# Optimization experiments

Hardware: AMD Instinct MI355X
Metric: run time of the kernel (lower is better)

## Reference

```python
import jax, jax.numpy as jnp
import numpy as np

N = 50000      # nodes
E = 800000     # edges
D = 128        # in_channels
H = 128        # hidden_channels
G = 64         # graphs in batch
OUT = 10       # out_channels
L = 6          # gcn layers (hardcoded in module)
EPS = 1e-5     # batchnorm eps


def setup_inputs() -> dict:
    key = jax.random.key(0)
    ks = jax.random.split(key, 8)
    s = 1.0 / np.sqrt(H)
    return {
        "x": jax.random.normal(ks[0], (N, D), jnp.float32),
        "edge_index": jax.random.randint(ks[1], (2, E), 0, N),
        "batch": jnp.sort(jax.random.randint(ks[2], (N,), 0, G)),
        "conv_W": jax.random.normal(ks[3], (L, D, H), jnp.float32) * s,
        "conv_b": jnp.zeros((L, H), jnp.float32),
        "bn_gamma": jnp.ones((L - 1, H), jnp.float32),
        "bn_beta": jnp.zeros((L - 1, H), jnp.float32),
        "head_W1": jax.random.normal(ks[4], (H, H), jnp.float32) * s,
        "head_b1": jnp.zeros((H,), jnp.float32),
        "head_bn_gamma": jnp.ones((H,), jnp.float32),
        "head_bn_beta": jnp.zeros((H,), jnp.float32),
        "head_W2": jax.random.normal(ks[5], (H, H), jnp.float32) * s,
        "head_b2": jnp.zeros((H,), jnp.float32),
        "head_W3": jax.random.normal(ks[6], (H, OUT), jnp.float32) * s,
        "head_b3": jnp.zeros((OUT,), jnp.float32),
    }


def _batchnorm(h, gamma, beta):
    # track_running_stats=False -> always batch statistics, biased variance
    mu = h.mean(axis=0)
    var = jnp.mean((h - mu) ** 2, axis=0)
    return (h - mu) * jax.lax.rsqrt(var + EPS) * gamma + beta


def reference(x, edge_index, batch, conv_W, conv_b, bn_gamma, bn_beta,
              head_W1, head_b1, head_bn_gamma, head_bn_beta,
              head_W2, head_b2, head_W3, head_b3):
    src, dst = edge_index[0], edge_index[1]
    # GCN symmetric norm with self-loops: deg = in-degree + 1
    deg = jnp.zeros((N,), x.dtype).at[dst].add(1.0) + 1.0
    dinv = jax.lax.rsqrt(deg)                 # deg^{-1/2}
    enorm = (dinv[src] * dinv[dst])[:, None]  # [E,1] edge weights
    self_w = (dinv * dinv)[:, None]           # [N,1] self-loop weight = 1/deg

    h = x
    for i in range(L):
        h = h @ conv_W[i]                                     # [N,H]
        agg = jnp.zeros_like(h).at[dst].add(h[src] * enorm)   # scatter-add
        h = agg + h * self_w + conv_b[i]
        if i < L - 1:
            h = jax.nn.relu(_batchnorm(h, bn_gamma[i], bn_beta[i]))
            # dropout(p=0.1) -> identity in eval

    # global_mean_pool over graphs
    counts = jnp.zeros((G,), h.dtype).at[batch].add(1.0)
    pooled = jnp.zeros((G, H), h.dtype).at[batch].add(h)
    pooled = pooled / jnp.clip(counts, 1.0)[:, None]

    # prediction head: Linear -> BN -> ReLU -> (Dropout) -> Linear -> ReLU -> Linear
    z = pooled @ head_W1 + head_b1
    z = jax.nn.relu(_batchnorm(z, head_bn_gamma, head_bn_beta))
    z = jax.nn.relu(z @ head_W2 + head_b2)
    return z @ head_W3 + head_b3
```

## Files before the change

### kernel.cpp

```cpp
#include <hip/hip_runtime.h>

#define N 50000
#define E 800000
#define H 128
#define G 64
#define OUTC 10
#define L 6
#define EPS 1e-5f

typedef unsigned short ushort_t;
typedef __attribute__((ext_vector_type(8))) short short8;
typedef __attribute__((ext_vector_type(8))) unsigned short ushort8;
typedef __attribute__((ext_vector_type(4))) float floatx4;

__device__ __forceinline__ void atomAddF(float* p, float v) {
  unsafeAtomicAdd(p, v);
}

__device__ __forceinline__ unsigned short f2bf(float f) {
  unsigned u = __float_as_uint(f);
  unsigned r = (u + 0x7FFF + ((u >> 16) & 1)) >> 16;
  return (unsigned short)r;
}
__device__ __forceinline__ float bf2f(unsigned short b) {
  return __uint_as_float(((unsigned)b) << 16);
}

__global__ void zero_kernel(int* __restrict__ p, int n) {
  int i = blockIdx.x * blockDim.x + threadIdx.x;
  if (i < n) p[i] = 0;
}

__global__ void deg_count_kernel(const int* __restrict__ dst, int* __restrict__ deg) {
  int e = blockIdx.x * blockDim.x + threadIdx.x;
  if (e < E) atomicAdd(&deg[dst[e]], 1);
}

__global__ void dinv_kernel(const int* __restrict__ deg, float* __restrict__ dinv) {
  int n = blockIdx.x * blockDim.x + threadIdx.x;
  if (n < N) dinv[n] = rsqrtf((float)(deg[n] + 1));
}

__global__ void prep_kernel(const float* __restrict__ x, const float* __restrict__ convW,
                            ushort_t* __restrict__ xb, ushort_t* __restrict__ WT) {
  int i = blockIdx.x * 256 + threadIdx.x;
  if (i < N * H) {
    xb[i] = f2bf(x[i]);
  } else {
    int j = i - N * H;
    if (j < L * H * H) {
      int l = j >> 14, r = j & 16383;
      int n = r >> 7, k = r & 127;
      WT[j] = f2bf(convW[l * 16384 + k * 128 + n]);
    }
  }
}

#define SCAN_B ((N + 255) / 256)

__global__ __launch_bounds__(256) void scanA_kernel(const int* __restrict__ deg,
                                                    int* __restrict__ blocksum) {
  __shared__ int red[256];
  int i = blockIdx.x * 256 + threadIdx.x;
  int v = (i < N) ? deg[i] : 0;
  red[threadIdx.x] = v;
  __syncthreads();
  for (int off = 128; off > 0; off >>= 1) {
    if (threadIdx.x < off) red[threadIdx.x] += red[threadIdx.x + off];
    __syncthreads();
  }
  if (threadIdx.x == 0) blocksum[blockIdx.x] = red[0];
}

__global__ __launch_bounds__(256) void scanB_kernel(int* __restrict__ blocksum) {
  __shared__ int sh[256];
  int t = threadIdx.x;
  sh[t] = (t < SCAN_B) ? blocksum[t] : 0;
  __syncthreads();
  for (int off = 1; off < 256; off <<= 1) {
    int v = (t >= off) ? sh[t - off] : 0;
    __syncthreads();
    sh[t] += v;
    __syncthreads();
  }
  if (t < SCAN_B) blocksum[t] = (t == 0) ? 0 : sh[t - 1];
}

__global__ __launch_bounds__(256) void scanC_kernel(const int* __restrict__ deg,
                                                    const int* __restrict__ blocksum,
                                                    int* __restrict__ rowptr) {
  __shared__ int sh[256];
  int i = blockIdx.x * 256 + threadIdx.x;
  int t = threadIdx.x;
  int d = (i < N) ? deg[i] : 0;
  sh[t] = d;
  __syncthreads();
  for (int off = 1; off < 256; off <<= 1) {
    int v = (t >= off) ? sh[t - off] : 0;
    __syncthreads();
    sh[t] += v;
    __syncthreads();
  }
  if (i < N) rowptr[i] = blocksum[blockIdx.x] + sh[t] - d;
  if (i == 0) rowptr[N] = E;
}

__global__ void csr_fill_kernel(const int* __restrict__ src, const int* __restrict__ dst,
                                const int* __restrict__ rowptr,
                                int* __restrict__ cursor, int* __restrict__ csr) {
  int e = blockIdx.x * blockDim.x + threadIdx.x;
  if (e < E) {
    int d = dst[e];
    int pos = rowptr[d] + atomicAdd(&cursor[d], 1);
    csr[pos] = src[e];
  }
}

__global__ void cnt_kernel(const int* __restrict__ batch, float* __restrict__ cnt) {
  __shared__ int lb[G + 1];
  int t = threadIdx.x;
  if (t <= G) {
    int lo = 0, hi = N;
    while (lo < hi) { int m = (lo + hi) >> 1; if (batch[m] < t) lo = m + 1; else hi = m; }
    lb[t] = lo;
  }
  __syncthreads();
  if (t < G) cnt[t] = (float)(lb[t + 1] - lb[t]);
}

__global__ __launch_bounds__(256) void gemm_mfma_kernel(
    const ushort_t* __restrict__ Ab, const ushort_t* __restrict__ WT,
    const float* __restrict__ dinv, ushort_t* __restrict__ hWs,
    const float* __restrict__ bnsums, const float* __restrict__ gamma,
    const float* __restrict__ beta)
{
  const int tid = threadIdx.x;
  const int wave = tid >> 6, lane = tid & 63;
  const int quad = lane >> 4, m = lane & 15;
  const int row0 = blockIdx.x * 64 + wave * 16;
  const int arow = min(row0 + m, N - 1);
  const float invN = 1.0f / (float)N;

  short8 afrag[4];
#pragma unroll
  for (int kc = 0; kc < 4; ++kc) {
    ushort8 raw = *(const ushort8*)&Ab[arow * H + kc * 32 + quad * 8];
    if (bnsums) {
      const int k0 = kc * 32 + quad * 8;
#pragma unroll
      for (int j = 0; j < 8; ++j) {
        float s = bnsums[k0 + j], q = bnsums[128 + k0 + j];
        float mu = s * invN;
        float var = q * invN - mu * mu;
        float rs = rsqrtf(var + EPS);
        float sc = gamma[k0 + j] * rs;
        float sh = beta[k0 + j] - mu * sc;
        raw[j] = f2bf(fmaxf(bf2f(raw[j]) * sc + sh, 0.f));
      }
    }
    short8 a;
#pragma unroll
    for (int j = 0; j < 8; ++j) a[j] = (short)raw[j];
    afrag[kc] = a;
  }

  float dv[4];
#pragma unroll
  for (int i = 0; i < 4; ++i) {
    int r = row0 + quad * 4 + i;
    dv[i] = (r < N) ? dinv[r] : 0.f;
  }

  const short* WTs = (const short*)WT;
#pragma unroll
  for (int nt = 0; nt < 8; ++nt) {
    floatx4 acc = {0.f, 0.f, 0.f, 0.f};
#pragma unroll
    for (int kc = 0; kc < 4; ++kc) {
      short8 bfrag = *(const short8*)&WTs[(nt * 16 + m) * H + kc * 32 + quad * 8];
      acc = __builtin_amdgcn_mfma_f32_16x16x32_bf16(afrag[kc], bfrag, acc, 0, 0, 0);
    }
    int col = nt * 16 + m;
#pragma unroll
    for (int i = 0; i < 4; ++i) {
      int r = row0 + quad * 4 + i;
      if (r < N) hWs[r * H + col] = f2bf(acc[i] * dv[i]);
    }
  }
}

__global__ __launch_bounds__(256) void gather_kernel(
    const ushort_t* __restrict__ hWs, const int* __restrict__ csr,
    const int* __restrict__ rowptr, const float* __restrict__ dinv,
    const float* __restrict__ bias, ushort_t* __restrict__ aggb)
{
  int t = blockIdx.x * 256 + threadIdx.x;
  int n = t >> 4, c8 = (t & 15) * 8;

  ushort8 us = *(const ushort8*)&hWs[n * H + c8];
  float acc[8];
#pragma unroll
  for (int j = 0; j < 8; ++j) acc[j] = bf2f(us[j]);

  int e = rowptr[n], end = rowptr[n + 1];
  for (; e + 3 < end; e += 4) {
    int s0 = csr[e], s1 = csr[e + 1], s2 = csr[e + 2], s3 = csr[e + 3];
    ushort8 u0 = *(const ushort8*)&hWs[s0 * H + c8];
    ushort8 u1 = *(const ushort8*)&hWs[s1 * H + c8];
    ushort8 u2 = *(const ushort8*)&hWs[s2 * H + c8];
    ushort8 u3 = *(const ushort8*)&hWs[s3 * H + c8];
#pragma unroll
    for (int j = 0; j < 8; ++j)
      acc[j] += (bf2f(u0[j]) + bf2f(u1[j])) + (bf2f(u2[j]) + bf2f(u3[j]));
  }
  for (; e < end; ++e) {
    int s0 = csr[e];
    ushort8 u0 = *(const ushort8*)&hWs[s0 * H + c8];
#pragma unroll
    for (int j = 0; j < 8; ++j) acc[j] += bf2f(u0[j]);
  }

  float dn = dinv[n];
  float4 b0 = *(const float4*)&bias[c8];
  float4 b1 = *(const float4*)&bias[c8 + 4];
  float bb[8] = {b0.x, b0.y, b0.z, b0.w, b1.x, b1.y, b1.z, b1.w};
  ushort8 o;
#pragma unroll
  for (int j = 0; j < 8; ++j) o[j] = f2bf(acc[j] * dn + bb[j]);
  *(ushort8*)&aggb[n * H + c8] = o;
}

__global__ __launch_bounds__(256) void bn_stats_kernel(
    const ushort_t* __restrict__ a, float* __restrict__ sums)
{
  __shared__ float red[256];
  int tid = threadIdx.x;
  int c = tid & 127, half = tid >> 7;
  int r0 = blockIdx.x * 128;
  float s = 0.f, q = 0.f;
  for (int i = 0; i < 64; ++i) {
    int r = r0 + i * 2 + half;
    if (r < N) { float v = bf2f(a[r * H + c]); s += v; q += v * v; }
  }
  red[tid] = s; __syncthreads();
  float s2 = (half == 0) ? s + red[tid + 128] : 0.f;
  __syncthreads();
  red[tid] = q; __syncthreads();
  if (half == 0) {
    float q2 = q + red[tid + 128];
    atomAddF(&sums[c], s2);
    atomAddF(&sums[128 + c], q2);
  }
}

__global__ __launch_bounds__(256) void pool_kernel(
    const ushort_t* __restrict__ h, const int* __restrict__ batch,
    float* __restrict__ pooled )
{
  int r0 = blockIdx.x * 128;
  int rend = min(r0 + 128, N);
  int c = threadIdx.x & 127, half = threadIdx.x >> 7;
  float acc = 0.f;
  int curg = -1;
  for (int r = r0 + half; r < rend; r += 2) {
    int g = batch[r];
    if (g != curg) {
      if (curg >= 0) atomAddF(&pooled[curg * H + c], acc);
      acc = 0.f; curg = g;
    }
    acc += bf2f(h[r * H + c]);
  }
  if (curg >= 0) atomAddF(&pooled[curg * H + c], acc);
}

__global__ void head1_kernel(const float* __restrict__ pooled, const float* __restrict__ cnt,
                             const float* __restrict__ W1, const float* __restrict__ b1,
                             float* __restrict__ z1)
{
  int t = blockIdx.x * 256 + threadIdx.x;
  int g = t >> 7, c = t & 127;
  float s = 0.f;
  for (int k = 0; k < H; ++k) s += pooled[g * H + k] * W1[k * H + c];
  z1[t] = s / fmaxf(cnt[g], 1.0f) + b1[c];
}

__global__ void head_bn_kernel(float* __restrict__ z1,
                               const float* __restrict__ gamma, const float* __restrict__ beta)
{
  int c = threadIdx.x;
  float s = 0.f, q = 0.f;
  for (int g = 0; g < G; ++g) { float v = z1[g * H + c]; s += v; q += v * v; }
  float mu = s / (float)G;
  float var = q / (float)G - mu * mu;
  float rs = rsqrtf(var + EPS);
  float ga = gamma[c], be = beta[c];
  for (int g = 0; g < G; ++g) {
    float v = z1[g * H + c];
    z1[g * H + c] = fmaxf((v - mu) * rs * ga + be, 0.f);
  }
}

__global__ void head2_kernel(const float* __restrict__ z1, const float* __restrict__ W2,
                             const float* __restrict__ b2, float* __restrict__ z2)
{
  int t = blockIdx.x * 256 + threadIdx.x;
  int g = t >> 7, c = t & 127;
  float s = b2[c];
  for (int k = 0; k < H; ++k) s += z1[g * H + k] * W2[k * H + c];
  z2[t] = fmaxf(s, 0.f);
}

__global__ void head3_kernel(const float* __restrict__ z2, const float* __restrict__ W3,
                             const float* __restrict__ b3, float* __restrict__ out)
{
  int t = blockIdx.x * 256 + threadIdx.x;
  if (t < G * OUTC) {
    int g = t / OUTC, o = t % OUTC;
    float s = b3[o];
    for (int k = 0; k < H; ++k) s += z2[g * H + k] * W3[k * OUTC + o];
    out[t] = s;
  }
}

extern "C" void kernel_launch(void* const* d_in, const int* in_sizes, int n_in,
                              void* d_out, int out_size, void* d_ws, size_t ws_size,
                              hipStream_t stream) {
  const float* x     = (const float*)d_in[0];
  const int*   ei    = (const int*)d_in[1];
  const int*   srcp  = ei;
  const int*   dstp  = ei + E;
  const int*   batch = (const int*)d_in[2];
  const float* convW = (const float*)d_in[3];
  const float* convb = (const float*)d_in[4];
  const float* bng   = (const float*)d_in[5];
  const float* bnb   = (const float*)d_in[6];
  const float* W1    = (const float*)d_in[7];
  const float* b1    = (const float*)d_in[8];
  const float* hg    = (const float*)d_in[9];
  const float* hb    = (const float*)d_in[10];
  const float* W2    = (const float*)d_in[11];
  const float* b2    = (const float*)d_in[12];
  const float* W3    = (const float*)d_in[13];
  const float* b3    = (const float*)d_in[14];
  float* out = (float*)d_out;

  const size_t NH2 = (size_t)N * H / 2;
  float*    ws     = (float*)d_ws;
  ushort_t* xb     = (ushort_t*)ws;
  ushort_t* aggb   = (ushort_t*)(ws + NH2);
  ushort_t* hWs    = (ushort_t*)(ws + 2 * NH2);
  ushort_t* WT     = (ushort_t*)(ws + 3 * NH2);
  float*    dinv   = ws + 3 * NH2 + (L * H * H / 2);
  int*      rowptr = (int*)(dinv + N);
  int*      csr    = rowptr + N + 1;
  int*      deg    = csr + E;
  int*      cursor = deg + N;
  float*    bnsums = (float*)(cursor + N);
  float*    pooled = bnsums + (L - 1) * 256;
  float*    cnt    = pooled + G * H;
  float*    z1     = cnt + G;
  float*    z2     = z1 + G * H;
  int*      bsum   = (int*)(z2 + G * H);

  const int zero_words = N + N + (L - 1) * 256 + G * H;
  zero_kernel<<<(zero_words + 255) / 256, 256, 0, stream>>>(deg, zero_words);
  deg_count_kernel<<<(E + 255) / 256, 256, 0, stream>>>(dstp, deg);
  dinv_kernel<<<(N + 255) / 256, 256, 0, stream>>>(deg, dinv);
  scanA_kernel<<<SCAN_B, 256, 0, stream>>>(deg, bsum);
  scanB_kernel<<<1, 256, 0, stream>>>(bsum);
  scanC_kernel<<<SCAN_B, 256, 0, stream>>>(deg, bsum, rowptr);
  csr_fill_kernel<<<(E + 255) / 256, 256, 0, stream>>>(srcp, dstp, rowptr, cursor, csr);
  cnt_kernel<<<1, 128, 0, stream>>>(batch, cnt);
  prep_kernel<<<(N * H + L * H * H + 255) / 256, 256, 0, stream>>>(x, convW, xb, WT);

  for (int l = 0; l < L; ++l) {
    const ushort_t* Ab = (l == 0) ? xb : aggb;
    const float* bs = (l == 0) ? nullptr : bnsums + (l - 1) * 256;
    const float* ga = (l == 0) ? nullptr : bng + (size_t)(l - 1) * H;
    const float* be = (l == 0) ? nullptr : bnb + (size_t)(l - 1) * H;
    gemm_mfma_kernel<<<(N + 63) / 64, 256, 0, stream>>>(
        Ab, WT + (size_t)l * H * H, dinv, hWs, bs, ga, be);
    gather_kernel<<<N * 16 / 256, 256, 0, stream>>>(
        hWs, csr, rowptr, dinv, convb + (size_t)l * H, aggb);
    if (l < L - 1)
      bn_stats_kernel<<<(N + 127) / 128, 256, 0, stream>>>(aggb, bnsums + l * 256);
  }

  pool_kernel<<<(N + 127) / 128, 256, 0, stream>>>(aggb, batch, pooled);
  head1_kernel<<<32, 256, 0, stream>>>(pooled, cnt, W1, b1, z1);
  head_bn_kernel<<<1, 128, 0, stream>>>(z1, hg, hb);
  head2_kernel<<<32, 256, 0, stream>>>(z1, W2, b2, z2);
  head3_kernel<<<3, 256, 0, stream>>>(z2, W3, b3, out);
}
```

Baseline: 714.1 us.

## Cut launch count, store aggregates in fp32, fuse head and scan kernels

Several small kernels are merged: the dinv computation moves into scanA, scanB is absorbed into scanC (each block reduces the preceding block sums itself), and the count, head1, head_bn, head2 and head3 kernels become one single-block head kernel. The zero kernel becomes hipMemsetAsync, and the x-to-bf16 conversion pass is dropped so the GEMM reads fp32 directly. Aggregated activations are now written and read as fp32 instead of bf16, which doubles that traffic in gather, bn_stats and the next GEMM but improves precision. The gather loop gains an 8-way unrolled path for more memory-level parallelism.

```diff
diff --git a/kernel.cpp b/kernel.cpp
--- a/kernel.cpp
+++ b/kernel.cpp
@@ -26,43 +26,29 @@
   return __uint_as_float(((unsigned)b) << 16);
 }
 
-__global__ void zero_kernel(int* __restrict__ p, int n) {
-  int i = blockIdx.x * blockDim.x + threadIdx.x;
-  if (i < n) p[i] = 0;
-}
-
 __global__ void deg_count_kernel(const int* __restrict__ dst, int* __restrict__ deg) {
   int e = blockIdx.x * blockDim.x + threadIdx.x;
   if (e < E) atomicAdd(&deg[dst[e]], 1);
 }
 
-__global__ void dinv_kernel(const int* __restrict__ deg, float* __restrict__ dinv) {
-  int n = blockIdx.x * blockDim.x + threadIdx.x;
-  if (n < N) dinv[n] = rsqrtf((float)(deg[n] + 1));
-}
-
-__global__ void prep_kernel(const float* __restrict__ x, const float* __restrict__ convW,
-                            ushort_t* __restrict__ xb, ushort_t* __restrict__ WT) {
-  int i = blockIdx.x * 256 + threadIdx.x;
-  if (i < N * H) {
-    xb[i] = f2bf(x[i]);
-  } else {
-    int j = i - N * H;
-    if (j < L * H * H) {
-      int l = j >> 14, r = j & 16383;
-      int n = r >> 7, k = r & 127;
-      WT[j] = f2bf(convW[l * 16384 + k * 128 + n]);
-    }
+__global__ void prep_kernel(const float* __restrict__ convW, ushort_t* __restrict__ WT) {
+  int j = blockIdx.x * 256 + threadIdx.x;
+  if (j < L * H * H) {
+    int l = j >> 14, r = j & 16383;
+    int n = r >> 7, k = r & 127;
+    WT[j] = f2bf(convW[l * 16384 + k * 128 + n]);
   }
 }
 
 #define SCAN_B ((N + 255) / 256)
 
 __global__ __launch_bounds__(256) void scanA_kernel(const int* __restrict__ deg,
-                                                    int* __restrict__ blocksum) {
+                                                    int* __restrict__ blocksum,
+                                                    float* __restrict__ dinv) {
   __shared__ int red[256];
   int i = blockIdx.x * 256 + threadIdx.x;
   int v = (i < N) ? deg[i] : 0;
+  if (i < N) dinv[i] = rsqrtf((float)(v + 1));
   red[threadIdx.x] = v;
   __syncthreads();
   for (int off = 128; off > 0; off >>= 1) {
@@ -72,10 +58,22 @@
   if (threadIdx.x == 0) blocksum[blockIdx.x] = red[0];
 }
 
-__global__ __launch_bounds__(256) void scanB_kernel(int* __restrict__ blocksum) {
+__global__ __launch_bounds__(256) void scanC_kernel(const int* __restrict__ deg,
+                                                    const int* __restrict__ blocksum,
+                                                    int* __restrict__ rowptr) {
+  __shared__ int pre[256];
   __shared__ int sh[256];
-  int t = threadIdx.x;
-  sh[t] = (t < SCAN_B) ? blocksum[t] : 0;
+  const int bid = blockIdx.x, t = threadIdx.x;
+  pre[t] = (t < bid) ? blocksum[t] : 0;
+  __syncthreads();
+  for (int off = 128; off > 0; off >>= 1) {
+    if (t < off) pre[t] += pre[t + off];
+    __syncthreads();
+  }
+  int base = pre[0];
+  int i = bid * 256 + t;
+  int d = (i < N) ? deg[i] : 0;
+  sh[t] = d;
   __syncthreads();
   for (int off = 1; off < 256; off <<= 1) {
     int v = (t >= off) ? sh[t - off] : 0;
@@ -83,25 +81,7 @@
     sh[t] += v;
     __syncthreads();
   }
-  if (t < SCAN_B) blocksum[t] = (t == 0) ? 0 : sh[t - 1];
-}
-
-__global__ __launch_bounds__(256) void scanC_kernel(const int* __restrict__ deg,
-                                                    const int* __restrict__ blocksum,
-                                                    int* __restrict__ rowptr) {
-  __shared__ int sh[256];
-  int i = blockIdx.x * 256 + threadIdx.x;
-  int t = threadIdx.x;
-  int d = (i < N) ? deg[i] : 0;
-  sh[t] = d;
-  __syncthreads();
-  for (int off = 1; off < 256; off <<= 1) {
-    int v = (t >= off) ? sh[t - off] : 0;
-    __syncthreads();
-    sh[t] += v;
-    __syncthreads();
-  }
-  if (i < N) rowptr[i] = blocksum[blockIdx.x] + sh[t] - d;
+  if (i < N) rowptr[i] = base + sh[t] - d;
   if (i == 0) rowptr[N] = E;
 }
 
@@ -116,20 +96,8 @@
   }
 }
 
-__global__ void cnt_kernel(const int* __restrict__ batch, float* __restrict__ cnt) {
-  __shared__ int lb[G + 1];
-  int t = threadIdx.x;
-  if (t <= G) {
-    int lo = 0, hi = N;
-    while (lo < hi) { int m = (lo + hi) >> 1; if (batch[m] < t) lo = m + 1; else hi = m; }
-    lb[t] = lo;
-  }
-  __syncthreads();
-  if (t < G) cnt[t] = (float)(lb[t + 1] - lb[t]);
-}
-
 __global__ __launch_bounds__(256) void gemm_mfma_kernel(
-    const ushort_t* __restrict__ Ab, const ushort_t* __restrict__ WT,
+    const float* __restrict__ A, const ushort_t* __restrict__ WT,
     const float* __restrict__ dinv, ushort_t* __restrict__ hWs,
     const float* __restrict__ bnsums, const float* __restrict__ gamma,
     const float* __restrict__ beta)
@@ -144,9 +112,11 @@
   short8 afrag[4];
 #pragma unroll
   for (int kc = 0; kc < 4; ++kc) {
-    ushort8 raw = *(const ushort8*)&Ab[arow * H + kc * 32 + quad * 8];
+    const int k0 = kc * 32 + quad * 8;
+    float4 f0 = *(const float4*)&A[arow * H + k0];
+    float4 f1 = *(const float4*)&A[arow * H + k0 + 4];
+    float vals[8] = {f0.x, f0.y, f0.z, f0.w, f1.x, f1.y, f1.z, f1.w};
     if (bnsums) {
-      const int k0 = kc * 32 + quad * 8;
 #pragma unroll
       for (int j = 0; j < 8; ++j) {
         float s = bnsums[k0 + j], q = bnsums[128 + k0 + j];
@@ -155,12 +125,12 @@
         float rs = rsqrtf(var + EPS);
         float sc = gamma[k0 + j] * rs;
         float sh = beta[k0 + j] - mu * sc;
-        raw[j] = f2bf(fmaxf(bf2f(raw[j]) * sc + sh, 0.f));
+        vals[j] = fmaxf(vals[j] * sc + sh, 0.f);
       }
     }
     short8 a;
 #pragma unroll
-    for (int j = 0; j < 8; ++j) a[j] = (short)raw[j];
+    for (int j = 0; j < 8; ++j) a[j] = (short)f2bf(vals[j]);
     afrag[kc] = a;
   }
 
@@ -192,7 +162,7 @@
 __global__ __launch_bounds__(256) void gather_kernel(
     const ushort_t* __restrict__ hWs, const int* __restrict__ csr,
     const int* __restrict__ rowptr, const float* __restrict__ dinv,
-    const float* __restrict__ bias, ushort_t* __restrict__ aggb)
+    const float* __restrict__ bias, float* __restrict__ agg)
 {
   int t = blockIdx.x * 256 + threadIdx.x;
   int n = t >> 4, c8 = (t & 15) * 8;
@@ -203,6 +173,22 @@
   for (int j = 0; j < 8; ++j) acc[j] = bf2f(us[j]);
 
   int e = rowptr[n], end = rowptr[n + 1];
+  for (; e + 7 < end; e += 8) {
+    int s0 = csr[e], s1 = csr[e + 1], s2 = csr[e + 2], s3 = csr[e + 3];
+    int s4 = csr[e + 4], s5 = csr[e + 5], s6 = csr[e + 6], s7 = csr[e + 7];
+    ushort8 u0 = *(const ushort8*)&hWs[s0 * H + c8];
+    ushort8 u1 = *(const ushort8*)&hWs[s1 * H + c8];
+    ushort8 u2 = *(const ushort8*)&hWs[s2 * H + c8];
+    ushort8 u3 = *(const ushort8*)&hWs[s3 * H + c8];
+    ushort8 u4 = *(const ushort8*)&hWs[s4 * H + c8];
+    ushort8 u5 = *(const ushort8*)&hWs[s5 * H + c8];
+    ushort8 u6 = *(const ushort8*)&hWs[s6 * H + c8];
+    ushort8 u7 = *(const ushort8*)&hWs[s7 * H + c8];
+#pragma unroll
+    for (int j = 0; j < 8; ++j)
+      acc[j] += ((bf2f(u0[j]) + bf2f(u1[j])) + (bf2f(u2[j]) + bf2f(u3[j]))) +
+                ((bf2f(u4[j]) + bf2f(u5[j])) + (bf2f(u6[j]) + bf2f(u7[j])));
+  }
   for (; e + 3 < end; e += 4) {
     int s0 = csr[e], s1 = csr[e + 1], s2 = csr[e + 2], s3 = csr[e + 3];
     ushort8 u0 = *(const ushort8*)&hWs[s0 * H + c8];
@@ -224,14 +210,16 @@
   float4 b0 = *(const float4*)&bias[c8];
   float4 b1 = *(const float4*)&bias[c8 + 4];
   float bb[8] = {b0.x, b0.y, b0.z, b0.w, b1.x, b1.y, b1.z, b1.w};
-  ushort8 o;
-#pragma unroll
-  for (int j = 0; j < 8; ++j) o[j] = f2bf(acc[j] * dn + bb[j]);
-  *(ushort8*)&aggb[n * H + c8] = o;
+  float4 o0 = make_float4(acc[0] * dn + bb[0], acc[1] * dn + bb[1],
+                          acc[2] * dn + bb[2], acc[3] * dn + bb[3]);
+  float4 o1 = make_float4(acc[4] * dn + bb[4], acc[5] * dn + bb[5],
+                          acc[6] * dn + bb[6], acc[7] * dn + bb[7]);
+  *(float4*)&agg[n * H + c8] = o0;
+  *(float4*)&agg[n * H + c8 + 4] = o1;
 }
 
 __global__ __launch_bounds__(256) void bn_stats_kernel(
-    const ushort_t* __restrict__ a, float* __restrict__ sums)
+    const float* __restrict__ a, float* __restrict__ sums)
 {
   __shared__ float red[256];
   int tid = threadIdx.x;
@@ -240,7 +228,7 @@
   float s = 0.f, q = 0.f;
   for (int i = 0; i < 64; ++i) {
     int r = r0 + i * 2 + half;
-    if (r < N) { float v = bf2f(a[r * H + c]); s += v; q += v * v; }
+    if (r < N) { float v = a[r * H + c]; s += v; q += v * v; }
   }
   red[tid] = s; __syncthreads();
   float s2 = (half == 0) ? s + red[tid + 128] : 0.f;
@@ -254,7 +242,7 @@
 }
 
 __global__ __launch_bounds__(256) void pool_kernel(
-    const ushort_t* __restrict__ h, const int* __restrict__ batch,
+    const float* __restrict__ h, const int* __restrict__ batch,
     float* __restrict__ pooled )
 {
   int r0 = blockIdx.x * 128;
@@ -268,57 +256,87 @@
       if (curg >= 0) atomAddF(&pooled[curg * H + c], acc);
       acc = 0.f; curg = g;
     }
-    acc += bf2f(h[r * H + c]);
+    acc += h[r * H + c];
   }
   if (curg >= 0) atomAddF(&pooled[curg * H + c], acc);
 }
 
-__global__ void head1_kernel(const float* __restrict__ pooled, const float* __restrict__ cnt,
-                             const float* __restrict__ W1, const float* __restrict__ b1,
-                             float* __restrict__ z1)
+__global__ __launch_bounds__(256) void head_kernel(
+    const float* __restrict__ pooled, const int* __restrict__ batch,
+    const float* __restrict__ W1, const float* __restrict__ b1,
+    const float* __restrict__ hg, const float* __restrict__ hb,
+    const float* __restrict__ W2, const float* __restrict__ b2,
+    const float* __restrict__ W3, const float* __restrict__ b3,
+    float* __restrict__ out)
 {
-  int t = blockIdx.x * 256 + threadIdx.x;
-  int g = t >> 7, c = t & 127;
-  float s = 0.f;
-  for (int k = 0; k < H; ++k) s += pooled[g * H + k] * W1[k * H + c];
-  z1[t] = s / fmaxf(cnt[g], 1.0f) + b1[c];
-}
-
-__global__ void head_bn_kernel(float* __restrict__ z1,
-                               const float* __restrict__ gamma, const float* __restrict__ beta)
-{
-  int c = threadIdx.x;
-  float s = 0.f, q = 0.f;
-  for (int g = 0; g < G; ++g) { float v = z1[g * H + c]; s += v; q += v * v; }
-  float mu = s / (float)G;
-  float var = q / (float)G - mu * mu;
-  float rs = rsqrtf(var + EPS);
-  float ga = gamma[c], be = beta[c];
-  for (int g = 0; g < G; ++g) {
-    float v = z1[g * H + c];
-    z1[g * H + c] = fmaxf((v - mu) * rs * ga + be, 0.f);
-  }
-}
-
-__global__ void head2_kernel(const float* __restrict__ z1, const float* __restrict__ W2,
-                             const float* __restrict__ b2, float* __restrict__ z2)
-{
-  int t = blockIdx.x * 256 + threadIdx.x;
-  int g = t >> 7, c = t & 127;
-  float s = b2[c];
-  for (int k = 0; k < H; ++k) s += z1[g * H + k] * W2[k * H + c];
-  z2[t] = fmaxf(s, 0.f);
-}
-
-__global__ void head3_kernel(const float* __restrict__ z2, const float* __restrict__ W3,
-                             const float* __restrict__ b3, float* __restrict__ out)
-{
-  int t = blockIdx.x * 256 + threadIdx.x;
-  if (t < G * OUTC) {
-    int g = t / OUTC, o = t % OUTC;
+  __shared__ float pl[G * H];
+  __shared__ float z1[G * H];
+  __shared__ float z2[G * H];
+  __shared__ int lb[G + 1];
+  const int t = threadIdx.x;
+
+  if (t <= G) {
+    int lo = 0, hi = N;
+    while (lo < hi) { int m2 = (lo + hi) >> 1; if (batch[m2] < t) lo = m2 + 1; else hi = m2; }
+    lb[t] = lo;
+  }
+  __syncthreads();
+
+  for (int i = t; i < G * H; i += 256) {
+    int g = i >> 7;
+    float c = (float)(lb[g + 1] - lb[g]);
+    pl[i] = pooled[i] / fmaxf(c, 1.0f);
+  }
+  __syncthreads();
+
+  const int c = t & 127, half = t >> 7;
+  {
+    float acc[32];
+#pragma unroll
+    for (int i = 0; i < 32; ++i) acc[i] = 0.f;
+    for (int k = 0; k < H; ++k) {
+      float w = W1[k * H + c];
+#pragma unroll
+      for (int i = 0; i < 32; ++i) acc[i] += pl[(half + 2 * i) * H + k] * w;
+    }
+    float bv = b1[c];
+#pragma unroll
+    for (int i = 0; i < 32; ++i) z1[(half + 2 * i) * H + c] = acc[i] + bv;
+  }
+  __syncthreads();
+
+  if (t < H) {
+    float s = 0.f, q = 0.f;
+    for (int g = 0; g < G; ++g) { float v = z1[g * H + t]; s += v; q += v * v; }
+    float mu = s / (float)G;
+    float var = q / (float)G - mu * mu;
+    float rs = rsqrtf(var + EPS);
+    float sc = hg[t] * rs, sh = hb[t] - mu * sc;
+    for (int g = 0; g < G; ++g)
+      z1[g * H + t] = fmaxf(z1[g * H + t] * sc + sh, 0.f);
+  }
+  __syncthreads();
+
+  {
+    float acc[32];
+#pragma unroll
+    for (int i = 0; i < 32; ++i) acc[i] = 0.f;
+    for (int k = 0; k < H; ++k) {
+      float w = W2[k * H + c];
+#pragma unroll
+      for (int i = 0; i < 32; ++i) acc[i] += z1[(half + 2 * i) * H + k] * w;
+    }
+    float bv = b2[c];
+#pragma unroll
+    for (int i = 0; i < 32; ++i) z2[(half + 2 * i) * H + c] = fmaxf(acc[i] + bv, 0.f);
+  }
+  __syncthreads();
+
+  for (int i = t; i < G * OUTC; i += 256) {
+    int g = i / OUTC, o = i % OUTC;
     float s = b3[o];
     for (int k = 0; k < H; ++k) s += z2[g * H + k] * W3[k * OUTC + o];
-    out[t] = s;
+    out[i] = s;
   }
 }
 
@@ -344,51 +362,40 @@
   const float* b3    = (const float*)d_in[14];
   float* out = (float*)d_out;
 
-  const size_t NH2 = (size_t)N * H / 2;
   float*    ws     = (float*)d_ws;
-  ushort_t* xb     = (ushort_t*)ws;
-  ushort_t* aggb   = (ushort_t*)(ws + NH2);
-  ushort_t* hWs    = (ushort_t*)(ws + 2 * NH2);
-  ushort_t* WT     = (ushort_t*)(ws + 3 * NH2);
-  float*    dinv   = ws + 3 * NH2 + (L * H * H / 2);
+  float*    agg    = ws;
+  ushort_t* hWs    = (ushort_t*)(agg + (size_t)N * H);
+  ushort_t* WT     = hWs + (size_t)N * H;
+  float*    dinv   = (float*)(WT + (size_t)L * H * H);
   int*      rowptr = (int*)(dinv + N);
   int*      csr    = rowptr + N + 1;
   int*      deg    = csr + E;
   int*      cursor = deg + N;
   float*    bnsums = (float*)(cursor + N);
   float*    pooled = bnsums + (L - 1) * 256;
-  float*    cnt    = pooled + G * H;
-  float*    z1     = cnt + G;
-  float*    z2     = z1 + G * H;
-  int*      bsum   = (int*)(z2 + G * H);
-
-  const int zero_words = N + N + (L - 1) * 256 + G * H;
-  zero_kernel<<<(zero_words + 255) / 256, 256, 0, stream>>>(deg, zero_words);
+  int*      bsum   = (int*)(pooled + G * H);
+
+  const size_t zero_bytes = (size_t)(N + N + (L - 1) * 256 + G * H) * 4;
+  hipMemsetAsync(deg, 0, zero_bytes, stream);
   deg_count_kernel<<<(E + 255) / 256, 256, 0, stream>>>(dstp, deg);
-  dinv_kernel<<<(N + 255) / 256, 256, 0, stream>>>(deg, dinv);
-  scanA_kernel<<<SCAN_B, 256, 0, stream>>>(deg, bsum);
-  scanB_kernel<<<1, 256, 0, stream>>>(bsum);
+  scanA_kernel<<<SCAN_B, 256, 0, stream>>>(deg, bsum, dinv);
   scanC_kernel<<<SCAN_B, 256, 0, stream>>>(deg, bsum, rowptr);
   csr_fill_kernel<<<(E + 255) / 256, 256, 0, stream>>>(srcp, dstp, rowptr, cursor, csr);
-  cnt_kernel<<<1, 128, 0, stream>>>(batch, cnt);
-  prep_kernel<<<(N * H + L * H * H + 255) / 256, 256, 0, stream>>>(x, convW, xb, WT);
+  prep_kernel<<<(L * H * H + 255) / 256, 256, 0, stream>>>(convW, WT);
 
   for (int l = 0; l < L; ++l) {
-    const ushort_t* Ab = (l == 0) ? xb : aggb;
+    const float* A  = (l == 0) ? x : agg;
     const float* bs = (l == 0) ? nullptr : bnsums + (l - 1) * 256;
     const float* ga = (l == 0) ? nullptr : bng + (size_t)(l - 1) * H;
     const float* be = (l == 0) ? nullptr : bnb + (size_t)(l - 1) * H;
     gemm_mfma_kernel<<<(N + 63) / 64, 256, 0, stream>>>(
-        Ab, WT + (size_t)l * H * H, dinv, hWs, bs, ga, be);
+        A, WT + (size_t)l * H * H, dinv, hWs, bs, ga, be);
     gather_kernel<<<N * 16 / 256, 256, 0, stream>>>(
-        hWs, csr, rowptr, dinv, convb + (size_t)l * H, aggb);
+        hWs, csr, rowptr, dinv, convb + (size_t)l * H, agg);
     if (l < L - 1)
-      bn_stats_kernel<<<(N + 127) / 128, 256, 0, stream>>>(aggb, bnsums + l * 256);
-  }
-
-  pool_kernel<<<(N + 127) / 128, 256, 0, stream>>>(aggb, batch, pooled);
-  head1_kernel<<<32, 256, 0, stream>>>(pooled, cnt, W1, b1, z1);
-  head_bn_kernel<<<1, 128, 0, stream>>>(z1, hg, hb);
-  head2_kernel<<<32, 256, 0, stream>>>(z1, W2, b2, z2);
-  head3_kernel<<<3, 256, 0, stream>>>(z2, W3, b3, out);
-}
+      bn_stats_kernel<<<(N + 127) / 128, 256, 0, stream>>>(agg, bnsums + l * 256);
+  }
+
+  pool_kernel<<<(N + 127) / 128, 256, 0, stream>>>(agg, batch, pooled);
+  head_kernel<<<1, 256, 0, stream>>>(pooled, batch, W1, b1, hg, hb, W2, b2, W3, b3, out);
+}
```

New measurement: 760.3 us. +6.5%, slower.
